# Optimization experiments

Measured on AMD Instinct MI355X. Metric: run time of the kernel, lower is better.

## Reference

```python
import jax, jax.numpy as jnp
import numpy as np

N_NODES = 100000
HIDDEN = 128
N_EDGES = 1000000


def setup_inputs() -> dict:
    key = jax.random.key(0)
    k1, k2, k3 = jax.random.split(key, 3)
    z = jax.random.normal(k1, (N_NODES, HIDDEN), dtype=jnp.float32)
    edge_index = jax.random.randint(k2, (2, N_EDGES), 0, N_NODES, dtype=jnp.int64)
    # xavier_uniform for square matrix: bound = sqrt(6/(fan_in+fan_out))
    bound = float(np.sqrt(6.0 / (HIDDEN + HIDDEN)))
    weights = jax.random.uniform(k3, (HIDDEN, HIDDEN), dtype=jnp.float32,
                                 minval=-bound, maxval=bound)
    return {"z": z, "edge_index": edge_index, "weights": weights}


def reference(z, edge_index, weights):
    # symm=True: symmetrize the bilinear form
    W = weights + weights.T                      # [d, d]
    z_src = z[edge_index[0]]                     # [E, d] gather
    z_dst = z[edge_index[1]]                     # [E, d] gather
    # torch: (W @ z_dst.T).T == z_dst @ W.T
    value = jnp.einsum('ed,dk,ek->e', z_src, W, z_dst)  # row-wise bilinear score
    return jax.nn.sigmoid(value)
```

## Files before the change

kernel.cpp:

```cpp
#include <hip/hip_runtime.h>

#define HIDDEN 128
#define LDSW 136
#define BSHIFT 5
#define NBMAX 3136
#define CAP 448
#define OVF_MAX 16384

typedef _Float16 f16;
typedef f16 f16x2 __attribute__((ext_vector_type(2)));
typedef f16 f16x8 __attribute__((ext_vector_type(8)));
typedef float f32x16 __attribute__((ext_vector_type(16)));
typedef unsigned long long ull;

static __device__ __forceinline__ float fdot2(f16x2 a, f16x2 b, float c) {
    return __builtin_amdgcn_fdot2(a, b, c, false);
}

__global__ __launch_bounds__(256) void prep_w(const float* __restrict__ w,
                                              f16* __restrict__ wsh_t,
                                              int* __restrict__ cursor,
                                              int* __restrict__ ovf_cnt,
                                              int nb) {
    int idx = blockIdx.x * 256 + threadIdx.x;
    if (idx < nb) cursor[idx] = idx * CAP;
    if (idx == nb) ovf_cnt[0] = 0;
    int n = idx >> 7, k = idx & 127;
    wsh_t[idx] = (f16)(w[k * HIDDEN + n] + w[n * HIDDEN + k]);
}

__global__ __launch_bounds__(256) void gemm_scatter(const float* __restrict__ z,
                                                    const f16* __restrict__ wsh_t,
                                                    f16* __restrict__ zh,
                                                    f16* __restrict__ uh,
                                                    const int* __restrict__ eidx,
                                                    int* __restrict__ cursor,
                                                    ull* __restrict__ perm,
                                                    ull* __restrict__ ovf,
                                                    int* __restrict__ ovf_cnt,
                                                    int nrows, int E, int nb, int ngemm) {
    __shared__ __align__(16) char smem[3 * NBMAX * 4];
    int tid = threadIdx.x;

    if (blockIdx.x >= ngemm) {
        int* lh    = (int*)smem;
        int* lbase = lh + NBMAX;
        int* lrank = lbase + NBMAX;
        int base = (blockIdx.x - ngemm) * 4096;
        for (int i = tid; i < nb; i += 256) { lh[i] = 0; lrank[i] = 0; }
        __syncthreads();
        int s[16], d[16], bb[16];
        #pragma unroll
        for (int i = 0; i < 16; ++i) {
            int e = base + i * 256 + tid;
            bb[i] = -1;
            if (e < E) {
                s[i] = eidx[e]; d[i] = eidx[E + e];
                bb[i] = d[i] >> BSHIFT;
                atomicAdd(&lh[bb[i]], 1);
            }
        }
        __syncthreads();
        for (int i = tid; i < nb; i += 256)
            if (lh[i]) lbase[i] = atomicAdd(&cursor[i], lh[i]);
        __syncthreads();
        #pragma unroll
        for (int i = 0; i < 16; ++i) {
            if (bb[i] >= 0) {
                int e = base + i * 256 + tid;
                int r = atomicAdd(&lrank[bb[i]], 1);
                long pos = (long)lbase[bb[i]] + r;
                ull v = (ull)s[i] | ((ull)d[i] << 17) | ((ull)e << 34);
                if (pos < (long)(bb[i] + 1) * CAP) perm[pos] = v;
                else {
                    int o = atomicAdd(ovf_cnt, 1);
                    if (o < OVF_MAX) ovf[o] = v;
                }
            }
        }
        return;
    }

    f16* wlt = (f16*)smem;
    {
        const f16x8* g = (const f16x8*)wsh_t;
        #pragma unroll
        for (int it = 0; it < 8; ++it) {
            int idx = it * 256 + tid;
            int j = idx >> 4, kc = idx & 15;
            *(f16x8*)&wlt[j * LDSW + kc * 8] = g[idx];
        }
    }
    __syncthreads();

    int wave = tid >> 6, lane = tid & 63;
    int row0 = blockIdx.x * 128 + wave * 32;
    if (row0 > nrows - 32) row0 = nrows - 32;

    int m = lane & 31, half = lane >> 5;
    const float* zr = z  + (size_t)(row0 + m) * HIDDEN + half * 8;
    f16*        zhr = zh + (size_t)(row0 + m) * HIDDEN + half * 8;
    const f16* wbase = &wlt[m * LDSW + half * 8];

    f32x16 acc0, acc1, acc2, acc3;
    #pragma unroll
    for (int r = 0; r < 16; ++r) { acc0[r] = 0.f; acc1[r] = 0.f; acc2[r] = 0.f; acc3[r] = 0.f; }

    #pragma unroll
    for (int ks = 0; ks < 8; ++ks) {
        float4 a0 = *(const float4*)(zr + 16 * ks);
        float4 a1 = *(const float4*)(zr + 16 * ks + 4);
        f16x8 af = {(f16)a0.x, (f16)a0.y, (f16)a0.z, (f16)a0.w,
                    (f16)a1.x, (f16)a1.y, (f16)a1.z, (f16)a1.w};
        *(f16x8*)(zhr + 16 * ks) = af;
        f16x8 b0 = *(const f16x8*)(wbase + 16 * ks);
        f16x8 b1 = *(const f16x8*)(wbase + 32 * LDSW + 16 * ks);
        f16x8 b2 = *(const f16x8*)(wbase + 64 * LDSW + 16 * ks);
        f16x8 b3 = *(const f16x8*)(wbase + 96 * LDSW + 16 * ks);
        acc0 = __builtin_amdgcn_mfma_f32_32x32x16_f16(af, b0, acc0, 0, 0, 0);
        acc1 = __builtin_amdgcn_mfma_f32_32x32x16_f16(af, b1, acc1, 0, 0, 0);
        acc2 = __builtin_amdgcn_mfma_f32_32x32x16_f16(af, b2, acc2, 0, 0, 0);
        acc3 = __builtin_amdgcn_mfma_f32_32x32x16_f16(af, b3, acc3, 0, 0, 0);
    }

    f16* ur = uh + (size_t)row0 * HIDDEN;
    #pragma unroll
    for (int r = 0; r < 16; ++r) {
        int row = (r & 3) + 8 * (r >> 2) + 4 * half;
        f16* p = ur + (size_t)row * HIDDEN + m;
        p[0]  = (f16)acc0[r];
        p[32] = (f16)acc1[r];
        p[64] = (f16)acc2[r];
        p[96] = (f16)acc3[r];
    }
}

static __device__ __forceinline__ void score_edge(const f16* uh, const f16* zh,
                                                  ull p, float* out, int t, int E) {
    int src = (int)(p & 0x1FFFF);
    int dst = (int)((p >> 17) & 0x1FFFF);
    int eid = (int)(p >> 34);
    const float4* a4 = (const float4*)(uh + (size_t)src * HIDDEN);
    const float4* b4 = (const float4*)(zh + (size_t)dst * HIDDEN);
    float4 av = a4[t], bv = b4[t];
    const f16x2* ap = (const f16x2*)&av;
    const f16x2* bp = (const f16x2*)&bv;
    float s = 0.f;
    #pragma unroll
    for (int i = 0; i < 4; ++i) s = fdot2(ap[i], bp[i], s);
    #pragma unroll
    for (int off = 8; off > 0; off >>= 1) s += __shfl_down(s, off, 16);
    if (t == 0 && eid < E) out[eid] = 1.0f / (1.0f + __expf(-s));
}

__global__ __launch_bounds__(1024) void edge_bin(const f16* __restrict__ uh,
                                                 const f16* __restrict__ zh,
                                                 const ull* __restrict__ perm,
                                                 const ull* __restrict__ ovf,
                                                 const int* __restrict__ ovf_cnt,
                                                 float* __restrict__ out,
                                                 int E, int cpb, int nb, int nmain) {
    int tid = threadIdx.x;
    int g = tid >> 4, t = tid & 15;
    int b = blockIdx.x;
    if (b >= nmain) {
        int n = ovf_cnt[0];
        if (n > OVF_MAX) n = OVF_MAX;
        for (int i = (b - nmain) * 64 + g; i < n; i += 32 * 64)
            score_edge(uh, zh, ovf[i], out, t, E);
        return;
    }
    int B = (b & 7) * cpb + (b >> 3);
    if (B >= nb) return;
    long base = (long)B * CAP;
    #pragma unroll 2
    for (int j = 0; j < CAP / 64; ++j)
        score_edge(uh, zh, perm[base + (long)j * 64 + g], out, t, E);
}

__global__ __launch_bounds__(256) void edge_score16(const f16* __restrict__ uh,
                                                    const f16* __restrict__ zh,
                                                    const int* __restrict__ eidx,
                                                    float* __restrict__ out, int E) {
    int tid = threadIdx.x;
    int g = tid >> 4, t = tid & 15;
    int e = blockIdx.x * 16 + g;
    if (e >= E) return;
    ull p = (ull)eidx[e] | ((ull)eidx[E + e] << 17) | ((ull)e << 34);
    score_edge(uh, zh, p, out, t, E);
}

extern "C" void kernel_launch(void* const* d_in, const int* in_sizes, int n_in,
                              void* d_out, int out_size, void* d_ws, size_t ws_size,
                              hipStream_t stream) {
    const float* z    = (const float*)d_in[0];
    const int*   eidx = (const int*)d_in[1];
    const float* w    = (const float*)d_in[2];
    float* out = (float*)d_out;

    int nrows = in_sizes[0] / HIDDEN;
    int E = out_size;
    int nb = ((nrows - 1) >> BSHIFT) + 1;

    f16* wsh_t  = (f16*)d_ws;
    f16* zh     = wsh_t + HIDDEN * HIDDEN;
    f16* uh     = zh + (size_t)nrows * HIDDEN;
    int* cursor = (int*)(uh + (size_t)nrows * HIDDEN);
    int* ovf_cnt = cursor + NBMAX;
    ull* ovf    = (ull*)(ovf_cnt + 2);
    ull* perm   = ovf + OVF_MAX;

    long nslots = (long)nb * CAP;
    size_t need = (size_t)((char*)(perm + nslots) - (char*)d_ws);
    bool binned = ws_size >= need;

    int ngemm = (nrows + 127) / 128;
    int nscat = (E + 4095) / 4096;

    prep_w<<<64, 256, 0, stream>>>(w, wsh_t, cursor, ovf_cnt, nb);
    if (binned) {
        gemm_scatter<<<ngemm + nscat, 256, 0, stream>>>(z, wsh_t, zh, uh, eidx, cursor,
                                                        perm, ovf, ovf_cnt, nrows, E, nb, ngemm);
        int cpb = (nb + 7) / 8;
        int nmain = 8 * cpb;
        edge_bin<<<nmain + 32, 1024, 0, stream>>>(uh, zh, perm, ovf, ovf_cnt, out,
                                                  E, cpb, nb, nmain);
    } else {
        gemm_scatter<<<ngemm, 256, 0, stream>>>(z, wsh_t, zh, uh, eidx, cursor,
                                                perm, ovf, ovf_cnt, nrows, E, nb, ngemm);
        edge_score16<<<(E + 15) / 16, 256, 0, stream>>>(uh, zh, eidx, out, E);
    }
}
```

Measured before the change: 178.4 us.

## Stage destination-bin rows in LDS and loop only over filled bin slots

The edge_bin kernel now copies the 32 destination rows of its bin from zh into shared memory and reads each edge's dst vector from LDS rather than global memory. It reads the bin's actual fill count from cursor and iterates only over occupied slots, so it no longer processes every CAP slot including padding. The block size drops from 1024 to 256 threads and CAP shrinks from 448 to 384, which cuts perm storage but may send more edges to the overflow path, and the overflow loop's stride changes to match. Edges that spill past the overflow cap, or bins with more edges than expected, are the main correctness risk.

```diff
diff --git a/kernel.cpp b/kernel.cpp
--- a/kernel.cpp
+++ b/kernel.cpp
@@ -3,8 +3,9 @@
 #define HIDDEN 128
 #define LDSW 136
 #define BSHIFT 5
+#define BS 32
 #define NBMAX 3136
-#define CAP 448
+#define CAP 384
 #define OVF_MAX 16384
 
 typedef _Float16 f16;
@@ -153,29 +154,56 @@
     if (t == 0 && eid < E) out[eid] = 1.0f / (1.0f + __expf(-s));
 }
 
-__global__ __launch_bounds__(1024) void edge_bin(const f16* __restrict__ uh,
-                                                 const f16* __restrict__ zh,
-                                                 const ull* __restrict__ perm,
-                                                 const ull* __restrict__ ovf,
-                                                 const int* __restrict__ ovf_cnt,
-                                                 float* __restrict__ out,
-                                                 int E, int cpb, int nb, int nmain) {
+__global__ __launch_bounds__(256) void edge_bin(const f16* __restrict__ uh,
+                                                const f16* __restrict__ zh,
+                                                const ull* __restrict__ perm,
+                                                const int* __restrict__ cursor,
+                                                const ull* __restrict__ ovf,
+                                                const int* __restrict__ ovf_cnt,
+                                                float* __restrict__ out,
+                                                int E, int cpb, int nb, int nmain) {
     int tid = threadIdx.x;
     int g = tid >> 4, t = tid & 15;
     int b = blockIdx.x;
     if (b >= nmain) {
         int n = ovf_cnt[0];
         if (n > OVF_MAX) n = OVF_MAX;
-        for (int i = (b - nmain) * 64 + g; i < n; i += 32 * 64)
+        for (int i = (b - nmain) * 16 + g; i < n; i += 32 * 16)
             score_edge(uh, zh, ovf[i], out, t, E);
         return;
     }
     int B = (b & 7) * cpb + (b >> 3);
     if (B >= nb) return;
+
+    __shared__ f16 dloc[BS * HIDDEN];
+    __shared__ int cnt_s;
+    {
+        const float4* zsrc = (const float4*)(zh + (size_t)B * BS * HIDDEN);
+        float4* dl = (float4*)dloc;
+        dl[tid]       = zsrc[tid];
+        dl[tid + 256] = zsrc[tid + 256];
+    }
+    if (tid == 0) cnt_s = cursor[B] - B * CAP;
+    __syncthreads();
+    int cnt = cnt_s; if (cnt > CAP) cnt = CAP;
+
     long base = (long)B * CAP;
-    #pragma unroll 2
-    for (int j = 0; j < CAP / 64; ++j)
-        score_edge(uh, zh, perm[base + (long)j * 64 + g], out, t, E);
+    for (int j = g; j < cnt; j += 16) {
+        ull p = perm[base + j];
+        int src = (int)(p & 0x1FFFF);
+        int dl  = (int)((p >> 17) & (BS - 1));
+        int eid = (int)(p >> 34);
+        float4 av = ((const float4*)(uh + (size_t)src * HIDDEN))[t];
+        f16x8  bv = *(const f16x8*)&dloc[dl * HIDDEN + t * 8];
+        const f16x2* ap = (const f16x2*)&av;
+        const f16x2* bp = (const f16x2*)&bv;
+        float s = 0.f;
+        #pragma unroll
+        for (int i = 0; i < 4; ++i) s = fdot2(ap[i], bp[i], s);
+        #pragma unroll
+        for (int off = 8; off > 0; off >>= 1) s += __shfl_down(s, off, 16);
+        if (t == 0 && eid < E) out[eid] = 1.0f / (1.0f + __expf(-s));
+    }
 }
 
 __global__ __launch_bounds__(256) void edge_score16(const f16* __restrict__ uh,
@@ -223,8 +251,8 @@
                                                         perm, ovf, ovf_cnt, nrows, E, nb, ngemm);
         int cpb = (nb + 7) / 8;
         int nmain = 8 * cpb;
-        edge_bin<<<nmain + 32, 1024, 0, stream>>>(uh, zh, perm, ovf, ovf_cnt, out,
-                                                  E, cpb, nb, nmain);
+        edge_bin<<<nmain + 32, 256, 0, stream>>>(uh, zh, perm, cursor, ovf, ovf_cnt, out,
+                                                 E, cpb, nb, nmain);
     } else {
         gemm_scatter<<<ngemm, 256, 0, stream>>>(z, wsh_t, zh, uh, eidx, cursor,
                                                 perm, ovf, ovf_cnt, nrows, E, nb, ngemm);
```

Measured after the change: 171.9 us. -3.6%, faster.
